# Optimization experiments

Hardware: AMD Instinct MI355X
Metric: run time of the kernel (lower is better)

Reference implementation:

```python
import jax, jax.numpy as jnp
import numpy as np

B, S, H, NH = 2, 2048, 128, 8  # batch, seq, num_hidden (= per-head dim), num_heads
LN_EPS = 1e-5


def _ln(x, g, b):
    m = jnp.mean(x, axis=-1, keepdims=True)
    v = jnp.var(x, axis=-1, keepdims=True)
    return (x - m) / jnp.sqrt(v + LN_EPS) * g + b


def setup_inputs() -> dict:
    key = jax.random.key(0)
    ks = jax.random.split(key, 18)
    sc = 0.02
    d = {}
    d["x"] = jax.random.normal(ks[0], (B, S, H), jnp.float32)
    # per-head full-dim projections, stacked over heads: [NH, H, H] (in->out layout)
    d["Wq"] = jax.random.normal(ks[1], (NH, H, H), jnp.float32) * sc
    d["bq"] = jax.random.normal(ks[2], (NH, H), jnp.float32) * sc
    d["Wk"] = jax.random.normal(ks[3], (NH, H, H), jnp.float32) * sc
    d["bk"] = jax.random.normal(ks[4], (NH, H), jnp.float32) * sc
    d["Wv"] = jax.random.normal(ks[5], (NH, H, H), jnp.float32) * sc
    d["bv"] = jax.random.normal(ks[6], (NH, H), jnp.float32) * sc
    d["Wo"] = jax.random.normal(ks[7], (NH * H, H), jnp.float32) * sc
    d["bo"] = jax.random.normal(ks[8], (H,), jnp.float32) * sc
    # conv1x1 FFN == pointwise linears: [H, 2H] and [2H, H]
    d["W1"] = jax.random.normal(ks[9], (H, 2 * H), jnp.float32) * sc
    d["b1"] = jax.random.normal(ks[10], (2 * H,), jnp.float32) * sc
    d["W2"] = jax.random.normal(ks[11], (2 * H, H), jnp.float32) * sc
    d["b2"] = jax.random.normal(ks[12], (H,), jnp.float32) * sc
    d["g1"] = jnp.ones((H,), jnp.float32)
    d["beta1"] = jnp.zeros((H,), jnp.float32)
    d["g2"] = jnp.ones((H,), jnp.float32)
    d["beta2"] = jnp.zeros((H,), jnp.float32)
    return d


def reference(x, Wq, bq, Wk, bk, Wv, bv, Wo, bo, W1, b1, W2, b2, g1, beta1, g2, beta2):
    # Multi-head attention: each head uses the FULL embed dim (faithful to source).
    Q = jnp.einsum('bsd,hde->bhse', x, Wq) + bq[None, :, None, :]
    K = jnp.einsum('bsd,hde->bhse', x, Wk) + bk[None, :, None, :]
    V = jnp.einsum('bsd,hde->bhse', x, Wv) + bv[None, :, None, :]
    scores = jnp.einsum('bhse,bhte->bhst', Q, K) / jnp.sqrt(jnp.float32(H))
    A = jax.nn.softmax(scores, axis=-1)          # [B, NH, S, S]
    o = jnp.einsum('bhst,bhte->bhse', A, V)      # [B, NH, S, H]
    o = o.transpose(0, 2, 1, 3).reshape(x.shape[0], x.shape[1], NH * H)  # concat heads
    y = o @ Wo + bo                               # W_O projection
    y = _ln(y, g1, beta1)                         # norm1 (no residual around attn, per source)
    f = jax.nn.relu(jax.nn.relu(y @ W1 + b1) @ W2 + b2)  # conv1x1 -> relu -> conv1x1 -> relu
    y = _ln(y + f, g2, beta2)                     # residual + norm2
    return y
```

## Files before the change

### kernel.cpp

```cpp
#include <hip/hip_runtime.h>
#include <math.h>

#define Bq  2
#define Sq  2048
#define Hq  128
#define NHq 8

typedef __attribute__((ext_vector_type(8))) short bf16x8;
typedef __attribute__((ext_vector_type(4))) float f32x4;
typedef __attribute__((ext_vector_type(16))) float f32x16;
typedef __attribute__((ext_vector_type(4))) unsigned short ushort4_t;
typedef __attribute__((ext_vector_type(4))) unsigned int uint4v;
typedef __attribute__((ext_vector_type(2))) unsigned long long u64x2;
typedef unsigned short ushort_t;
typedef unsigned int uint_t;
typedef unsigned long long u64;

__device__ inline ushort_t f2bf(float f) {
    union { float f; uint_t u; } c; c.f = f;
    uint_t u = c.u + 0x7FFFu + ((c.u >> 16) & 1u);
    return (ushort_t)(u >> 16);
}
__device__ inline float bf2f(ushort_t u) {
    union { uint_t u; float f; } c; c.u = ((uint_t)u) << 16;
    return c.f;
}

__device__ inline float exp2_fast(float x) {
    float r;
    asm("v_exp_f32 %0, %1" : "=v"(r) : "v"(x));
    return r;
}

__device__ inline uint_t cvtpk_bf16(float lo, float hi) {
    uint_t r;
    asm("v_cvt_pk_bf16_f32 %0, %1, %2" : "=v"(r) : "v"(lo), "v"(hi));
    return r;
}
__device__ inline void pswap32(uint_t &a, uint_t &b) {
    asm("v_permlane32_swap_b32 %0, %1" : "+v"(a), "+v"(b));
}

#define GLOAD16(gsrc, ldst) \
    __builtin_amdgcn_global_load_lds( \
        (const __attribute__((address_space(1))) unsigned int*)(const void*)(gsrc), \
        (__attribute__((address_space(3))) unsigned int*)(ldst), 16, 0, 0)

__global__ __launch_bounds__(256) void tw_kernel(
    const float* __restrict__ Wq, const float* __restrict__ Wk, const float* __restrict__ Wv,
    const float* __restrict__ Wo, const float* __restrict__ W1, const float* __restrict__ W2,
    const float* __restrict__ x,
    ushort_t* __restrict__ Wt_all, ushort_t* __restrict__ Wot,
    ushort_t* __restrict__ W1t, ushort_t* __restrict__ W2t, ushort_t* __restrict__ xb)
{
    const int z = blockIdx.y;
    const int t = threadIdx.x;

    if (z == 27) {
        const int r0 = blockIdx.x << 5;
        #pragma unroll
        for (int i = 0; i < 2; ++i) {
            const int c = t + i * 256;
            const int row = r0 + (c >> 4), j = (c & 15) * 8;
            const float* xp = x + (size_t)row * 128 + j;
            const float4 a = *(const float4*)xp;
            const float4 b = *(const float4*)(xp + 4);
            bf16x8 v;
            v[0]=f2bf(a.x); v[1]=f2bf(a.y); v[2]=f2bf(a.z); v[3]=f2bf(a.w);
            v[4]=f2bf(b.x); v[5]=f2bf(b.y); v[6]=f2bf(b.z); v[7]=f2bf(b.w);
            *(bf16x8*)&xb[(size_t)row * 128 + j] = v;
        }
        return;
    }

    const float* src; ushort_t* dst; int R, C;
    if (z < 24) { const int h = z & 7;
        src = (z < 8 ? Wq : z < 16 ? Wk : Wv) + h * 16384;
        dst = Wt_all + z * 16384; R = 128; C = 128;
    } else if (z == 24) { src = Wo; dst = Wot; R = 1024; C = 128; }
    else if (z == 25)   { src = W1; dst = W1t; R = 128;  C = 256; }
    else                { src = W2; dst = W2t; R = 256;  C = 128; }

    const int tpc = C >> 5;
    if ((int)blockIdx.x >= (R >> 5) * tpc) return;
    const int r0 = (blockIdx.x / tpc) << 5;
    const int c0 = (blockIdx.x % tpc) << 5;

    __shared__ float ls[32][33];
    const int lr = t >> 5, lc = t & 31;
    #pragma unroll
    for (int i = 0; i < 4; ++i)
        ls[lr + i * 8][lc] = src[(size_t)(r0 + lr + i * 8) * C + c0 + lc];
    __syncthreads();
    const int wc = t >> 3, wr0 = (t & 7) << 2;
    ushort4_t o4;
    o4[0] = f2bf(ls[wr0 + 0][wc]); o4[1] = f2bf(ls[wr0 + 1][wc]);
    o4[2] = f2bf(ls[wr0 + 2][wc]); o4[3] = f2bf(ls[wr0 + 3][wc]);
    *(ushort4_t*)&dst[(size_t)(c0 + wc) * R + r0 + wr0] = o4;
}

__global__ __launch_bounds__(256) void qkv_gemm(
    const ushort_t* __restrict__ xb, const ushort_t* __restrict__ Wt_all,
    const float* __restrict__ bq, const float* __restrict__ bk, const float* __restrict__ bv,
    ushort_t* __restrict__ Qb, ushort_t* __restrict__ Kb, ushort_t* __restrict__ Vb)
{
    __shared__ ushort_t As[64 * 128];
    __shared__ ushort_t Bs[128 * 128];
    const int tid = threadIdx.x;
    const int w = tid >> 6, l = tid & 63, lg = l >> 4, ln = l & 15;
    const int m0 = blockIdx.x << 6;

    #pragma unroll
    for (int i = 0; i < 4; ++i) {
        const int seg = w * 4 + i;
        const int row = seg * 4 + (l >> 4);
        const int j = (l & 15) ^ (row & 15);
        GLOAD16(xb + (size_t)(m0 + row) * 128 + j * 8, &As[seg * 512]);
    }

    bf16x8 af[4];

    #pragma unroll
    for (int half = 0; half < 2; ++half) {
        const int z = blockIdx.y + half * 12;
        const ushort_t* Wz = Wt_all + (size_t)z * 16384;
        #pragma unroll
        for (int i = 0; i < 8; ++i) {
            const int seg = w * 8 + i;
            const int row = seg * 4 + (l >> 4);
            const int j = (l & 15) ^ (row & 15);
            GLOAD16(Wz + row * 128 + j * 8, &Bs[seg * 512]);
        }
        __syncthreads();

        if (half == 0) {
            #pragma unroll
            for (int kc = 0; kc < 4; ++kc)
                af[kc] = *(const bf16x8*)&As[(w * 16 + ln) * 128 + (((kc * 4 + lg) ^ ln) << 3)];
        }

        f32x4 acc[8];
        #pragma unroll
        for (int nt = 0; nt < 8; ++nt) acc[nt] = (f32x4){0.f,0.f,0.f,0.f};
        #pragma unroll
        for (int nt = 0; nt < 8; ++nt)
            #pragma unroll
            for (int kc = 0; kc < 4; ++kc) {
                const bf16x8 bn = *(const bf16x8*)&Bs[(nt * 16 + ln) * 128 + (((kc * 4 + lg) ^ ln) << 3)];
                acc[nt] = __builtin_amdgcn_mfma_f32_16x16x32_bf16(af[kc], bn, acc[nt], 0, 0, 0);
            }

        const float* bias = (z < 8 ? bq : z < 16 ? bk : bv) + (z & 7) * 128;
        ushort_t* outp = (z < 8 ? Qb : z < 16 ? Kb : Vb);
        const float scale = z < 8 ? (0.08838834764831845f * 1.4426950408889634f) : 1.0f;
        const int h = z & 7;
        #pragma unroll
        for (int nt = 0; nt < 8; ++nt) {
            const float bb = bias[nt * 16 + ln];
            #pragma unroll
            for (int j2 = 0; j2 < 4; ++j2) {
                const int r = m0 + w * 16 + lg * 4 + j2;
                const int b = r >> 11, s = r & 2047;
                outp[((size_t)((b << 3) + h) * 2048 + s) * 128 + nt * 16 + ln] =
                    f2bf((acc[nt][j2] + bb) * scale);
            }
        }
        __syncthreads();
    }
}

__global__ __launch_bounds__(256, 2) void attn_kernel(
    const ushort_t* __restrict__ Q, const ushort_t* __restrict__ K,
    const ushort_t* __restrict__ V, ushort_t* __restrict__ Opart,
    float2* __restrict__ ml)
{
    __shared__ ushort_t sh[32768];
    ushort_t* Vt = sh + 16384;

    const int tid = threadIdx.x;
    const int w = tid >> 6, l = tid & 63;
    const int ln5 = l & 31, h5 = l >> 5;

    const int id  = blockIdx.x;
    const int id2 = (id & 7) * 64 + (id >> 3);
    const int s   = id2 >> 8;
    const int bh  = (id2 >> 4) & 15;
    const int q0  = (id2 & 15) << 7;
    const int kv0 = s << 10;

    const size_t base = (size_t)bh * Sq * Hq;
    const ushort_t* Qp = Q + base;
    const ushort_t* Kp = K + base + (size_t)kv0 * Hq;
    const ushort_t* Vp = V + base + (size_t)kv0 * Hq;

    bf16x8 qf[8];
    {
        const ushort_t* qrow = Qp + (size_t)(q0 + w * 32 + ln5) * Hq;
        #pragma unroll
        for (int kc = 0; kc < 8; ++kc)
            qf[kc] = *(const bf16x8*)(qrow + kc * 16 + h5 * 8);
    }

    const int kv2 = (tid & 31) * 2;
    const int d8  = (tid >> 5) * 8;

    f32x16 po[4];
    #pragma unroll
    for (int dt = 0; dt < 4; ++dt)
        #pragma unroll
        for (int r = 0; r < 16; ++r) po[dt][r] = 0.f;
    float m_ = -1e30f, l_ = 0.f;

    #pragma unroll
    for (int i = 0; i < 4; ++i) {
        const int seg = w * 4 + i;
        const int row = seg * 4 + (l >> 4);
        const int j = (l & 15) ^ (row & 15);
        GLOAD16(Kp + (size_t)row * Hq + j * 8, &sh[seg * 512]);
    }
    bf16x8 va0 = *(const bf16x8*)(Vp + (size_t)kv2 * Hq + d8);
    bf16x8 va1 = *(const bf16x8*)(Vp + (size_t)(kv2 + 1) * Hq + d8);
    bf16x8 vb0 = *(const bf16x8*)(Vp + (size_t)kv2 * Hq + d8 + 64);
    bf16x8 vb1 = *(const bf16x8*)(Vp + (size_t)(kv2 + 1) * Hq + d8 + 64);
    __syncthreads();
    #pragma unroll
    for (int jj = 0; jj < 8; ++jj) {
        const int r1 = d8 + jj, r2 = d8 + 64 + jj;
        *(uint_t*)&Vt[r1 * 128 + ((((kv2 >> 3) ^ (r1 & 15))) << 3) + (kv2 & 7)] =
            (uint_t)(ushort_t)va0[jj] | ((uint_t)(ushort_t)va1[jj] << 16);
        *(uint_t*)&Vt[r2 * 128 + ((((kv2 >> 3) ^ (r2 & 15))) << 3) + (kv2 & 7)] =
            (uint_t)(ushort_t)vb0[jj] | ((uint_t)(ushort_t)vb1[jj] << 16);
    }
    __syncthreads();

    const int NT = 1024 / 64;
    for (int t = 0; t < NT; ++t) {
        const int buf = t & 1;
        const ushort_t* Ksb = sh + buf * 8192;

        if (t + 1 < NT) {
            const int k0n = (t + 1) * 64;
            #pragma unroll
            for (int i = 0; i < 4; ++i) {
                const int seg = w * 4 + i;
                const int row = seg * 4 + (l >> 4);
                const int j = (l & 15) ^ (row & 15);
                GLOAD16(Kp + (size_t)(k0n + row) * Hq + j * 8, &sh[(buf ^ 1) * 8192 + seg * 512]);
            }
            va0 = *(const bf16x8*)(Vp + (size_t)(k0n + kv2) * Hq + d8);
            va1 = *(const bf16x8*)(Vp + (size_t)(k0n + kv2 + 1) * Hq + d8);
            vb0 = *(const bf16x8*)(Vp + (size_t)(k0n + kv2) * Hq + d8 + 64);
            vb1 = *(const bf16x8*)(Vp + (size_t)(k0n + kv2 + 1) * Hq + d8 + 64);
        }

        f32x16 st[2];
        #pragma unroll
        for (int mt = 0; mt < 2; ++mt)
            #pragma unroll
            for (int r = 0; r < 16; ++r) st[mt][r] = 0.f;

        __builtin_amdgcn_s_setprio(1);
        #pragma unroll
        for (int kc = 0; kc < 8; ++kc) {
            #pragma unroll
            for (int mt = 0; mt < 2; ++mt) {
                const int row = mt * 32 + ln5;
                const int slot = (kc * 2 + h5) ^ (row & 15);
                const bf16x8 ka = *(const bf16x8*)&Ksb[row * 128 + (slot << 3)];
                st[mt] = __builtin_amdgcn_mfma_f32_32x32x16_bf16(ka, qf[kc], st[mt], 0, 0, 0);
            }
        }
        __builtin_amdgcn_s_setprio(0);

        float mxv[16];
        #pragma unroll
        for (int r = 0; r < 16; ++r) mxv[r] = fmaxf(st[0][r], st[1][r]);
        #pragma unroll
        for (int sd = 8; sd >= 1; sd >>= 1)
            #pragma unroll
            for (int i = 0; i < sd; ++i) mxv[i] = fmaxf(mxv[i], mxv[i + sd]);
        float mx = mxv[0];
        mx = fmaxf(mx, __shfl_xor(mx, 32));

        const bool anyup = __any(mx > m_ + 8.0f);
        float sc = 1.0f;
        if (anyup) {
            const float mn = fmaxf(m_, mx);
            sc = exp2_fast(m_ - mn);
            m_ = mn;
        }

        float pe[32];
        #pragma unroll
        for (int mt = 0; mt < 2; ++mt)
            #pragma unroll
            for (int r = 0; r < 16; ++r)
                pe[mt * 16 + r] = exp2_fast(st[mt][r] - m_);

        float sv[16];
        #pragma unroll
        for (int r = 0; r < 16; ++r) sv[r] = pe[r] + pe[16 + r];
        #pragma unroll
        for (int sd = 8; sd >= 1; sd >>= 1)
            #pragma unroll
            for (int i = 0; i < sd; ++i) sv[i] += sv[i + sd];
        float rs = sv[0];
        rs += __shfl_xor(rs, 32);
        l_ = l_ * sc + rs;

        bf16x8 pb[4];
        #pragma unroll
        for (int ks = 0; ks < 4; ++ks) {
            const int o = (ks >> 1) * 16 + (ks & 1) * 8;
            uint_t wA = cvtpk_bf16(pe[o + 0], pe[o + 1]);
            uint_t wB = cvtpk_bf16(pe[o + 4], pe[o + 5]);
            pswap32(wA, wB);
            uint_t wC = cvtpk_bf16(pe[o + 2], pe[o + 3]);
            uint_t wD = cvtpk_bf16(pe[o + 6], pe[o + 7]);
            pswap32(wC, wD);
            uint4v wv; wv[0] = wA; wv[1] = wC; wv[2] = wB; wv[3] = wD;
            pb[ks] = __builtin_bit_cast(bf16x8, wv);
        }

        if (anyup) {
            #pragma unroll
            for (int dt = 0; dt < 4; ++dt)
                #pragma unroll
                for (int r = 0; r < 16; ++r) po[dt][r] *= sc;
        }

        __builtin_amdgcn_s_setprio(1);
        #pragma unroll
        for (int dt = 0; dt < 4; ++dt) {
            #pragma unroll
            for (int ks = 0; ks < 4; ++ks) {
                const int row = dt * 32 + ln5;
                const int slot = (ks * 2 + h5) ^ (row & 15);
                const bf16x8 va = *(const bf16x8*)&Vt[row * 128 + (slot << 3)];
                po[dt] = __builtin_amdgcn_mfma_f32_32x32x16_bf16(va, pb[ks], po[dt], 0, 0, 0);
            }
        }
        __builtin_amdgcn_s_setprio(0);

        __syncthreads();
        if (t + 1 < NT) {
            #pragma unroll
            for (int jj = 0; jj < 8; ++jj) {
                const int r1 = d8 + jj, r2 = d8 + 64 + jj;
                *(uint_t*)&Vt[r1 * 128 + ((((kv2 >> 3) ^ (r1 & 15))) << 3) + (kv2 & 7)] =
                    (uint_t)(ushort_t)va0[jj] | ((uint_t)(ushort_t)va1[jj] << 16);
                *(uint_t*)&Vt[r2 * 128 + ((((kv2 >> 3) ^ (r2 & 15))) << 3) + (kv2 & 7)] =
                    (uint_t)(ushort_t)vb0[jj] | ((uint_t)(ushort_t)vb1[jj] << 16);
            }
        }
        __syncthreads();
    }

    char* shb = (char*)sh;
    char* wb = shb + w * 8448;
    #pragma unroll
    for (int dt = 0; dt < 4; ++dt)
        #pragma unroll
        for (int r = 0; r < 16; r += 2) {
            const int d = dt * 32 + (r & 3) + 8 * (r >> 2) + 4 * h5;
            const uint_t pk = cvtpk_bf16(po[dt][r], po[dt][r + 1]);
            *(uint_t*)(wb + ln5 * 264 + d * 2) = pk;
        }
    const int rid0 = (s * 16 + bh) * 2048 + q0 + w * 32;
    #pragma unroll
    for (int rb = 0; rb < 8; ++rb) {
        const int qr = rb * 4 + (l >> 4);
        const char* rp = wb + qr * 264 + (l & 15) * 16;
        u64x2 vv;
        vv[0] = *(const u64*)rp;
        vv[1] = *(const u64*)(rp + 8);
        *(u64x2*)(Opart + (size_t)(rid0 + qr) * 128 + (l & 15) * 8) = vv;
    }
    if (h5 == 0)
        ml[rid0 + ln5] = make_float2(m_, l_);
}

__global__ __launch_bounds__(256) void wo_ln_kernel(
    const ushort_t* __restrict__ Opart, const float2* __restrict__ ml,
    const ushort_t* __restrict__ Wot, const float* __restrict__ bo,
    const float* __restrict__ g1, const float* __restrict__ be1,
    float* __restrict__ y, ushort_t* __restrict__ yb)
{
    __shared__ ushort_t As[32 * 128];
    __shared__ ushort_t Bs[128 * 128];
    __shared__ float ybuf[32 * 132];
    const int tid = threadIdx.x;
    const int w = tid >> 6, l = tid & 63, lg = l >> 4, ln = l & 15;
    const int m0 = blockIdx.x << 5;
    const int rw = (w & 1) * 16;
    const int cw = (w >> 1) * 4;

    f32x4 acc[4];
    #pragma unroll
    for (int nt = 0; nt < 4; ++nt) acc[nt] = (f32x4){0.f,0.f,0.f,0.f};

    for (int ks = 0; ks < 8; ++ks) {
        const int k0 = ks << 7;
        #pragma unroll
        for (int i = 0; i < 2; ++i) {
            const int c = tid + i * 256;
            const int row = c >> 4, j = c & 15;
            const int r = m0 + row, b = r >> 11, q = r & 2047;
            const int prow = ((b << 3) + ks) * 2048 + q;
            const float2 e0 = ml[prow];
            const float2 e1 = ml[32768 + prow];
            const float M = fmaxf(e0.x, e1.x);
            const float w0 = exp2_fast(e0.x - M), w1 = exp2_fast(e1.x - M);
            const float inv = 1.0f / (w0 * e0.y + w1 * e1.y);
            const size_t po_ = (size_t)prow * 128 + j * 8;
            const bf16x8 o0 = *(const bf16x8*)&Opart[po_];
            const bf16x8 o1 = *(const bf16x8*)&Opart[po_ + (size_t)32768 * 128];
            bf16x8 mv;
            #pragma unroll
            for (int jj = 0; jj < 8; ++jj) {
                const float v = (w0 * bf2f((ushort_t)o0[jj]) + w1 * bf2f((ushort_t)o1[jj])) * inv;
                mv[jj] = (short)f2bf(v);
            }
            *(bf16x8*)&As[row * 128 + ((j ^ (row & 15)) << 3)] = mv;
        }
        #pragma unroll
        for (int i = 0; i < 8; ++i) {
            const int seg = w * 8 + i;
            const int row = seg * 4 + (l >> 4);
            const int j = (l & 15) ^ (row & 15);
            GLOAD16(Wot + (size_t)row * 1024 + k0 + j * 8, &Bs[seg * 512]);
        }
        __syncthreads();

        bf16x8 af[4];
        #pragma unroll
        for (int kc = 0; kc < 4; ++kc)
            af[kc] = *(const bf16x8*)&As[(rw + ln) * 128 + (((kc * 4 + lg) ^ ln) << 3)];
        #pragma unroll
        for (int nt = 0; nt < 4; ++nt)
            #pragma unroll
            for (int kc = 0; kc < 4; ++kc) {
                const bf16x8 bn = *(const bf16x8*)&Bs[((cw + nt) * 16 + ln) * 128 + (((kc * 4 + lg) ^ ln) << 3)];
                acc[nt] = __builtin_amdgcn_mfma_f32_16x16x32_bf16(af[kc], bn, acc[nt], 0, 0, 0);
            }
        __syncthreads();
    }

    #pragma unroll
    for (int nt = 0; nt < 4; ++nt) {
        const int col = (cw + nt) * 16 + ln;
        const float bb = bo[col];
        #pragma unroll
        for (int j2 = 0; j2 < 4; ++j2)
            ybuf[(rw + lg * 4 + j2) * 132 + col] = acc[nt][j2] + bb;
    }
    __syncthreads();

    const int row = tid >> 3, sub = tid & 7;
    float vals[16];
    float sm = 0.f, sq = 0.f;
    #pragma unroll
    for (int e = 0; e < 16; ++e) {
        const float v = ybuf[row * 132 + sub * 16 + e];
        vals[e] = v; sm += v; sq += v * v;
    }
    #pragma unroll
    for (int mmk = 1; mmk <= 4; mmk <<= 1) {
        sm += __shfl_xor(sm, mmk);
        sq += __shfl_xor(sq, mmk);
    }
    const float mean = sm * (1.0f / 128.0f);
    const float var  = sq * (1.0f / 128.0f) - mean * mean;
    const float rstd = rsqrtf(var + 1e-5f);
    const int r = m0 + row;
    float* yp = y + (size_t)r * 128 + sub * 16;
    ushort_t* ybp = yb + (size_t)r * 128 + sub * 16;
    #pragma unroll
    for (int e = 0; e < 16; e += 2) {
        const int col = sub * 16 + e;
        const float v0 = (vals[e]   - mean) * rstd * g1[col]   + be1[col];
        const float v1 = (vals[e+1] - mean) * rstd * g1[col+1] + be1[col+1];
        yp[e] = v0; yp[e+1] = v1;
        *(uint_t*)&ybp[e] = (uint_t)f2bf(v0) | ((uint_t)f2bf(v1) << 16);
    }
}

__global__ __launch_bounds__(256) void ffn_fused_kernel(
    const ushort_t* __restrict__ yb, const ushort_t* __restrict__ W1t,
    const float* __restrict__ b1, const ushort_t* __restrict__ W2t,
    const float* __restrict__ b2, const float* __restrict__ y,
    const float* __restrict__ g2, const float* __restrict__ be2,
    float* __restrict__ out)
{
    __shared__ ushort_t As[32 * 128];
    __shared__ ushort_t Bs[128 * 128];
    __shared__ ushort_t Hs[2][32 * 128];
    __shared__ float ybuf[32 * 132];
    const int tid = threadIdx.x;
    const int w = tid >> 6, l = tid & 63, lg = l >> 4, ln = l & 15;
    const int m0 = blockIdx.x << 5;
    const int rw = (w & 1) * 16;
    const int cw = (w >> 1) * 4;

    #pragma unroll
    for (int i = 0; i < 2; ++i) {
        const int seg = w * 2 + i;
        const int row = seg * 4 + (l >> 4);
        const int j = (l & 15) ^ (row & 15);
        GLOAD16(yb + (size_t)(m0 + row) * 128 + j * 8, &As[seg * 512]);
    }

    bf16x8 af[4];
    #pragma unroll
    for (int half = 0; half < 2; ++half) {
        const int n0 = half << 7;
        #pragma unroll
        for (int i = 0; i < 8; ++i) {
            const int seg = w * 8 + i;
            const int row = seg * 4 + (l >> 4);
            const int j = (l & 15) ^ (row & 15);
            GLOAD16(W1t + (size_t)(n0 + row) * 128 + j * 8, &Bs[seg * 512]);
        }
        __syncthreads();

        if (half == 0) {
            #pragma unroll
            for (int kc = 0; kc < 4; ++kc)
                af[kc] = *(const bf16x8*)&As[(rw + ln) * 128 + (((kc * 4 + lg) ^ ln) << 3)];
        }

        f32x4 acc[4];
        #pragma unroll
        for (int nt = 0; nt < 4; ++nt) acc[nt] = (f32x4){0.f,0.f,0.f,0.f};
        #pragma unroll
        for (int nt = 0; nt < 4; ++nt)
            #pragma unroll
            for (int kc = 0; kc < 4; ++kc) {
                const bf16x8 bn = *(const bf16x8*)&Bs[((cw + nt) * 16 + ln) * 128 + (((kc * 4 + lg) ^ ln) << 3)];
                acc[nt] = __builtin_amdgcn_mfma_f32_16x16x32_bf16(af[kc], bn, acc[nt], 0, 0, 0);
            }

        #pragma unroll
        for (int nt = 0; nt < 4; ++nt) {
            const int colh = (cw + nt) * 16 + ln;
            const float bb = b1[n0 + colh];
            #pragma unroll
            for (int j2 = 0; j2 < 4; ++j2) {
                const int row = rw + lg * 4 + j2;
                const float v = fmaxf(acc[nt][j2] + bb, 0.f);
                Hs[half][row * 128 + ((((colh >> 3) ^ (row & 15))) << 3) + (colh & 7)] = f2bf(v);
            }
        }
        __syncthreads();
    }

    f32x4 acc2[4];
    #pragma unroll
    for (int nt = 0; nt < 4; ++nt) acc2[nt] = (f32x4){0.f,0.f,0.f,0.f};

    #pragma unroll
    for (int ks = 0; ks < 2; ++ks) {
        const int k0 = ks << 7;
        #pragma unroll
        for (int i = 0; i < 8; ++i) {
            const int seg = w * 8 + i;
            const int row = seg * 4 + (l >> 4);
            const int j = (l & 15) ^ (row & 15);
            GLOAD16(W2t + (size_t)row * 256 + k0 + j * 8, &Bs[seg * 512]);
        }
        __syncthreads();

        bf16x8 af2[4];
        #pragma unroll
        for (int kc = 0; kc < 4; ++kc)
            af2[kc] = *(const bf16x8*)&Hs[ks][(rw + ln) * 128 + (((kc * 4 + lg) ^ ln) << 3)];
        #pragma unroll
        for (int nt = 0; nt < 4; ++nt)
            #pragma unroll
            for (int kc = 0; kc < 4; ++kc) {
                const bf16x8 bn = *(const bf16x8*)&Bs[((cw + nt) * 16 + ln) * 128 + (((kc * 4 + lg) ^ ln) << 3)];
                acc2[nt] = __builtin_amdgcn_mfma_f32_16x16x32_bf16(af2[kc], bn, acc2[nt], 0, 0, 0);
            }
        __syncthreads();
    }

    #pragma unroll
    for (int nt = 0; nt < 4; ++nt) {
        const int col = (cw + nt) * 16 + ln;
        const float bb = b2[col];
        #pragma unroll
        for (int j2 = 0; j2 < 4; ++j2) {
            const int row = rw + lg * 4 + j2;
            const float f = fmaxf(acc2[nt][j2] + bb, 0.f);
            ybuf[row * 132 + col] = f + y[(size_t)(m0 + row) * 128 + col];
        }
    }
    __syncthreads();

    const int row = tid >> 3, sub = tid & 7;
    float vals[16];
    float sm = 0.f, sq = 0.f;
    #pragma unroll
    for (int e = 0; e < 16; ++e) {
        const float v = ybuf[row * 132 + sub * 16 + e];
        vals[e] = v; sm += v; sq += v * v;
    }
    #pragma unroll
    for (int mmk = 1; mmk <= 4; mmk <<= 1) {
        sm += __shfl_xor(sm, mmk);
        sq += __shfl_xor(sq, mmk);
    }
    const float mean = sm * (1.0f / 128.0f);
    const float var  = sq * (1.0f / 128.0f) - mean * mean;
    const float rstd = rsqrtf(var + 1e-5f);
    float* op = out + (size_t)(m0 + row) * 128 + sub * 16;
    #pragma unroll
    for (int e = 0; e < 16; ++e) {
        const int col = sub * 16 + e;
        op[e] = (vals[e] - mean) * rstd * g2[col] + be2[col];
    }
}

extern "C" void kernel_launch(void* const* d_in, const int* in_sizes, int n_in,
                              void* d_out, int out_size, void* d_ws, size_t ws_size,
                              hipStream_t stream)
{
    const float* x   = (const float*)d_in[0];
    const float* Wq  = (const float*)d_in[1];
    const float* bq  = (const float*)d_in[2];
    const float* Wk  = (const float*)d_in[3];
    const float* bk  = (const float*)d_in[4];
    const float* Wv  = (const float*)d_in[5];
    const float* bv  = (const float*)d_in[6];
    const float* Wo  = (const float*)d_in[7];
    const float* bo  = (const float*)d_in[8];
    const float* W1  = (const float*)d_in[9];
    const float* b1  = (const float*)d_in[10];
    const float* W2  = (const float*)d_in[11];
    const float* b2  = (const float*)d_in[12];
    const float* g1  = (const float*)d_in[13];
    const float* be1 = (const float*)d_in[14];
    const float* g2  = (const float*)d_in[15];
    const float* be2 = (const float*)d_in[16];
    (void)in_sizes; (void)n_in; (void)out_size; (void)ws_size;

    ushort_t* Wt_all = (ushort_t*)d_ws;
    ushort_t* Wot   = Wt_all + 393216;
    ushort_t* W1t   = Wot + 131072;
    ushort_t* W2t   = W1t + 32768;
    ushort_t* xb    = W2t + 32768;
    ushort_t* Qb    = xb + 524288;
    ushort_t* Kb    = Qb + 4194304;
    ushort_t* Vb    = Kb + 4194304;
    ushort_t* Opart = Vb + 4194304;
    float2*   ml    = (float2*)(Opart + 8388608);
    float*    y  = (float*)Qb;
    ushort_t* yb = Kb;

    tw_kernel    <<<dim3(128, 28), 256, 0, stream>>>(Wq, Wk, Wv, Wo, W1, W2, x,
                                                     Wt_all, Wot, W1t, W2t, xb);
    qkv_gemm     <<<dim3(64, 12),  256, 0, stream>>>(xb, Wt_all, bq, bk, bv, Qb, Kb, Vb);
    attn_kernel  <<<dim3(512),     256, 0, stream>>>(Qb, Kb, Vb, Opart, ml);
    wo_ln_kernel <<<dim3(128),     256, 0, stream>>>(Opart, ml, Wot, bo, g1, be1, y, yb);
    ffn_fused_kernel<<<dim3(128),  256, 0, stream>>>(yb, W1t, b1, W2t, b2, y,
                                                     g2, be2, (float*)d_out);
}
```

Measured before the change: 86.42 us.

## Fuse Wo+LN1 with FFN+LN2 kernel and reorder K prefetch after QK MFMA

Merges the output-projection/LayerNorm kernel with the FFN/LayerNorm kernel so the normalized activations stay in shared memory (ybuf and a swizzled bf16 tile) instead of round-tripping through global memory, and one kernel launch is removed. In the attention loop, the QK^T MFMA block now runs before issuing the next tile's K/V global loads, changing how loads overlap with compute. The fused kernel uses more shared memory per block, which may reduce occupancy, and the moved prefetch could expose load latency differently.

After: 82.60 us. -4.4%, faster.

```diff
diff --git a/kernel.cpp b/kernel.cpp
--- a/kernel.cpp
+++ b/kernel.cpp
@@ -238,6 +238,25 @@
         const int buf = t & 1;
         const ushort_t* Ksb = sh + buf * 8192;
 
+        f32x16 st[2];
+        #pragma unroll
+        for (int mt = 0; mt < 2; ++mt)
+            #pragma unroll
+            for (int r = 0; r < 16; ++r) st[mt][r] = 0.f;
+
+        __builtin_amdgcn_s_setprio(1);
+        #pragma unroll
+        for (int kc = 0; kc < 8; ++kc) {
+            #pragma unroll
+            for (int mt = 0; mt < 2; ++mt) {
+                const int row = mt * 32 + ln5;
+                const int slot = (kc * 2 + h5) ^ (row & 15);
+                const bf16x8 ka = *(const bf16x8*)&Ksb[row * 128 + (slot << 3)];
+                st[mt] = __builtin_amdgcn_mfma_f32_32x32x16_bf16(ka, qf[kc], st[mt], 0, 0, 0);
+            }
+        }
+        __builtin_amdgcn_s_setprio(0);
+
         if (t + 1 < NT) {
             const int k0n = (t + 1) * 64;
             #pragma unroll
@@ -252,25 +271,6 @@
             vb0 = *(const bf16x8*)(Vp + (size_t)(k0n + kv2) * Hq + d8 + 64);
             vb1 = *(const bf16x8*)(Vp + (size_t)(k0n + kv2 + 1) * Hq + d8 + 64);
         }
-
-        f32x16 st[2];
-        #pragma unroll
-        for (int mt = 0; mt < 2; ++mt)
-            #pragma unroll
-            for (int r = 0; r < 16; ++r) st[mt][r] = 0.f;
-
-        __builtin_amdgcn_s_setprio(1);
-        #pragma unroll
-        for (int kc = 0; kc < 8; ++kc) {
-            #pragma unroll
-            for (int mt = 0; mt < 2; ++mt) {
-                const int row = mt * 32 + ln5;
-                const int slot = (kc * 2 + h5) ^ (row & 15);
-                const bf16x8 ka = *(const bf16x8*)&Ksb[row * 128 + (slot << 3)];
-                st[mt] = __builtin_amdgcn_mfma_f32_32x32x16_bf16(ka, qf[kc], st[mt], 0, 0, 0);
-            }
-        }
-        __builtin_amdgcn_s_setprio(0);
 
         float mxv[16];
         #pragma unroll
@@ -380,14 +380,18 @@
         ml[rid0 + ln5] = make_float2(m_, l_);
 }
 
-__global__ __launch_bounds__(256) void wo_ln_kernel(
+__global__ __launch_bounds__(256) void wo_ffn_kernel(
     const ushort_t* __restrict__ Opart, const float2* __restrict__ ml,
     const ushort_t* __restrict__ Wot, const float* __restrict__ bo,
     const float* __restrict__ g1, const float* __restrict__ be1,
-    float* __restrict__ y, ushort_t* __restrict__ yb)
+    const ushort_t* __restrict__ W1t, const float* __restrict__ b1,
+    const ushort_t* __restrict__ W2t, const float* __restrict__ b2,
+    const float* __restrict__ g2, const float* __restrict__ be2,
+    float* __restrict__ out)
 {
     __shared__ ushort_t As[32 * 128];
     __shared__ ushort_t Bs[128 * 128];
+    __shared__ ushort_t Hs[2][32 * 128];
     __shared__ float ybuf[32 * 132];
     const int tid = threadIdx.x;
     const int w = tid >> 6, l = tid & 63, lg = l >> 4, ln = l & 15;
@@ -432,16 +436,16 @@
         }
         __syncthreads();
 
-        bf16x8 af[4];
+        bf16x8 af0[4];
         #pragma unroll
         for (int kc = 0; kc < 4; ++kc)
-            af[kc] = *(const bf16x8*)&As[(rw + ln) * 128 + (((kc * 4 + lg) ^ ln) << 3)];
+            af0[kc] = *(const bf16x8*)&As[(rw + ln) * 128 + (((kc * 4 + lg) ^ ln) << 3)];
         #pragma unroll
         for (int nt = 0; nt < 4; ++nt)
             #pragma unroll
             for (int kc = 0; kc < 4; ++kc) {
                 const bf16x8 bn = *(const bf16x8*)&Bs[((cw + nt) * 16 + ln) * 128 + (((kc * 4 + lg) ^ ln) << 3)];
-                acc[nt] = __builtin_amdgcn_mfma_f32_16x16x32_bf16(af[kc], bn, acc[nt], 0, 0, 0);
+                acc[nt] = __builtin_amdgcn_mfma_f32_16x16x32_bf16(af0[kc], bn, acc[nt], 0, 0, 0);
             }
         __syncthreads();
     }
@@ -456,59 +460,36 @@
     }
     __syncthreads();
 
-    const int row = tid >> 3, sub = tid & 7;
-    float vals[16];
-    float sm = 0.f, sq = 0.f;
-    #pragma unroll
-    for (int e = 0; e < 16; ++e) {
-        const float v = ybuf[row * 132 + sub * 16 + e];
-        vals[e] = v; sm += v; sq += v * v;
-    }
-    #pragma unroll
-    for (int mmk = 1; mmk <= 4; mmk <<= 1) {
-        sm += __shfl_xor(sm, mmk);
-        sq += __shfl_xor(sq, mmk);
-    }
-    const float mean = sm * (1.0f / 128.0f);
-    const float var  = sq * (1.0f / 128.0f) - mean * mean;
-    const float rstd = rsqrtf(var + 1e-5f);
-    const int r = m0 + row;
-    float* yp = y + (size_t)r * 128 + sub * 16;
-    ushort_t* ybp = yb + (size_t)r * 128 + sub * 16;
-    #pragma unroll
-    for (int e = 0; e < 16; e += 2) {
-        const int col = sub * 16 + e;
-        const float v0 = (vals[e]   - mean) * rstd * g1[col]   + be1[col];
-        const float v1 = (vals[e+1] - mean) * rstd * g1[col+1] + be1[col+1];
-        yp[e] = v0; yp[e+1] = v1;
-        *(uint_t*)&ybp[e] = (uint_t)f2bf(v0) | ((uint_t)f2bf(v1) << 16);
-    }
-}
-
-__global__ __launch_bounds__(256) void ffn_fused_kernel(
-    const ushort_t* __restrict__ yb, const ushort_t* __restrict__ W1t,
-    const float* __restrict__ b1, const ushort_t* __restrict__ W2t,
-    const float* __restrict__ b2, const float* __restrict__ y,
-    const float* __restrict__ g2, const float* __restrict__ be2,
-    float* __restrict__ out)
-{
-    __shared__ ushort_t As[32 * 128];
-    __shared__ ushort_t Bs[128 * 128];
-    __shared__ ushort_t Hs[2][32 * 128];
-    __shared__ float ybuf[32 * 132];
-    const int tid = threadIdx.x;
-    const int w = tid >> 6, l = tid & 63, lg = l >> 4, ln = l & 15;
-    const int m0 = blockIdx.x << 5;
-    const int rw = (w & 1) * 16;
-    const int cw = (w >> 1) * 4;
-
-    #pragma unroll
-    for (int i = 0; i < 2; ++i) {
-        const int seg = w * 2 + i;
-        const int row = seg * 4 + (l >> 4);
-        const int j = (l & 15) ^ (row & 15);
-        GLOAD16(yb + (size_t)(m0 + row) * 128 + j * 8, &As[seg * 512]);
-    }
+    {
+        const int row = tid >> 3, sub = tid & 7;
+        float vals[16];
+        float sm = 0.f, sq = 0.f;
+        #pragma unroll
+        for (int e = 0; e < 16; ++e) {
+            const float v = ybuf[row * 132 + sub * 16 + e];
+            vals[e] = v; sm += v; sq += v * v;
+        }
+        #pragma unroll
+        for (int mmk = 1; mmk <= 4; mmk <<= 1) {
+            sm += __shfl_xor(sm, mmk);
+            sq += __shfl_xor(sq, mmk);
+        }
+        const float mean = sm * (1.0f / 128.0f);
+        const float var  = sq * (1.0f / 128.0f) - mean * mean;
+        const float rstd = rsqrtf(var + 1e-5f);
+        #pragma unroll
+        for (int e = 0; e < 16; e += 2) {
+            const int col = sub * 16 + e;
+            const float v0 = (vals[e]   - mean) * rstd * g1[col]   + be1[col];
+            const float v1 = (vals[e+1] - mean) * rstd * g1[col+1] + be1[col+1];
+            ybuf[row * 132 + col]     = v0;
+            ybuf[row * 132 + col + 1] = v1;
+            const int jch = col >> 3;
+            *(uint_t*)&As[row * 128 + ((jch ^ (row & 15)) << 3) + (col & 7)] =
+                (uint_t)f2bf(v0) | ((uint_t)f2bf(v1) << 16);
+        }
+    }
+    __syncthreads();
 
     bf16x8 af[4];
     #pragma unroll
@@ -529,15 +510,15 @@
                 af[kc] = *(const bf16x8*)&As[(rw + ln) * 128 + (((kc * 4 + lg) ^ ln) << 3)];
         }
 
-        f32x4 acc[4];
-        #pragma unroll
-        for (int nt = 0; nt < 4; ++nt) acc[nt] = (f32x4){0.f,0.f,0.f,0.f};
+        f32x4 acc1[4];
+        #pragma unroll
+        for (int nt = 0; nt < 4; ++nt) acc1[nt] = (f32x4){0.f,0.f,0.f,0.f};
         #pragma unroll
         for (int nt = 0; nt < 4; ++nt)
             #pragma unroll
             for (int kc = 0; kc < 4; ++kc) {
                 const bf16x8 bn = *(const bf16x8*)&Bs[((cw + nt) * 16 + ln) * 128 + (((kc * 4 + lg) ^ ln) << 3)];
-                acc[nt] = __builtin_amdgcn_mfma_f32_16x16x32_bf16(af[kc], bn, acc[nt], 0, 0, 0);
+                acc1[nt] = __builtin_amdgcn_mfma_f32_16x16x32_bf16(af[kc], bn, acc1[nt], 0, 0, 0);
             }
 
         #pragma unroll
@@ -547,7 +528,7 @@
             #pragma unroll
             for (int j2 = 0; j2 < 4; ++j2) {
                 const int row = rw + lg * 4 + j2;
-                const float v = fmaxf(acc[nt][j2] + bb, 0.f);
+                const float v = fmaxf(acc1[nt][j2] + bb, 0.f);
                 Hs[half][row * 128 + ((((colh >> 3) ^ (row & 15))) << 3) + (colh & 7)] = f2bf(v);
             }
         }
@@ -592,32 +573,34 @@
         for (int j2 = 0; j2 < 4; ++j2) {
             const int row = rw + lg * 4 + j2;
             const float f = fmaxf(acc2[nt][j2] + bb, 0.f);
-            ybuf[row * 132 + col] = f + y[(size_t)(m0 + row) * 128 + col];
+            ybuf[row * 132 + col] = f + ybuf[row * 132 + col];
         }
     }
     __syncthreads();
 
-    const int row = tid >> 3, sub = tid & 7;
-    float vals[16];
-    float sm = 0.f, sq = 0.f;
-    #pragma unroll
-    for (int e = 0; e < 16; ++e) {
-        const float v = ybuf[row * 132 + sub * 16 + e];
-        vals[e] = v; sm += v; sq += v * v;
-    }
-    #pragma unroll
-    for (int mmk = 1; mmk <= 4; mmk <<= 1) {
-        sm += __shfl_xor(sm, mmk);
-        sq += __shfl_xor(sq, mmk);
-    }
-    const float mean = sm * (1.0f / 128.0f);
-    const float var  = sq * (1.0f / 128.0f) - mean * mean;
-    const float rstd = rsqrtf(var + 1e-5f);
-    float* op = out + (size_t)(m0 + row) * 128 + sub * 16;
-    #pragma unroll
-    for (int e = 0; e < 16; ++e) {
-        const int col = sub * 16 + e;
-        op[e] = (vals[e] - mean) * rstd * g2[col] + be2[col];
+    {
+        const int row = tid >> 3, sub = tid & 7;
+        float vals[16];
+        float sm = 0.f, sq = 0.f;
+        #pragma unroll
+        for (int e = 0; e < 16; ++e) {
+            const float v = ybuf[row * 132 + sub * 16 + e];
+            vals[e] = v; sm += v; sq += v * v;
+        }
+        #pragma unroll
+        for (int mmk = 1; mmk <= 4; mmk <<= 1) {
+            sm += __shfl_xor(sm, mmk);
+            sq += __shfl_xor(sq, mmk);
+        }
+        const float mean = sm * (1.0f / 128.0f);
+        const float var  = sq * (1.0f / 128.0f) - mean * mean;
+        const float rstd = rsqrtf(var + 1e-5f);
+        float* op = out + (size_t)(m0 + row) * 128 + sub * 16;
+        #pragma unroll
+        for (int e = 0; e < 16; ++e) {
+            const int col = sub * 16 + e;
+            op[e] = (vals[e] - mean) * rstd * g2[col] + be2[col];
+        }
     }
 }
 
@@ -654,14 +637,12 @@
     ushort_t* Vb    = Kb + 4194304;
     ushort_t* Opart = Vb + 4194304;
     float2*   ml    = (float2*)(Opart + 8388608);
-    float*    y  = (float*)Qb;
-    ushort_t* yb = Kb;
 
     tw_kernel    <<<dim3(128, 28), 256, 0, stream>>>(Wq, Wk, Wv, Wo, W1, W2, x,
                                                      Wt_all, Wot, W1t, W2t, xb);
     qkv_gemm     <<<dim3(64, 12),  256, 0, stream>>>(xb, Wt_all, bq, bk, bv, Qb, Kb, Vb);
     attn_kernel  <<<dim3(512),     256, 0, stream>>>(Qb, Kb, Vb, Opart, ml);
-    wo_ln_kernel <<<dim3(128),     256, 0, stream>>>(Opart, ml, Wot, bo, g1, be1, y, yb);
-    ffn_fused_kernel<<<dim3(128),  256, 0, stream>>>(yb, W1t, b1, W2t, b2, y,
-                                                     g2, be2, (float*)d_out);
-}
+    wo_ffn_kernel<<<dim3(128),     256, 0, stream>>>(Opart, ml, Wot, bo, g1, be1,
+                                                     W1t, b1, W2t, b2, g2, be2,
+                                                     (float*)d_out);
+}
```
